# Kernel optimization log

Measured on AMD Instinct MI355X. Metric: run time of the kernel, lower is better.

## Reference

```python
import jax, jax.numpy as jnp
import numpy as np

HIDDEN = 1024
FFN = 4096
N_EXPERTS = 8
TOP_K = 2


def setup_inputs() -> dict:
    key = jax.random.key(0)
    ks = jax.random.split(key, 6)
    x = jax.random.normal(ks[0], (2, 2048, HIDDEN), dtype=jnp.float32)
    Wr = jax.random.normal(ks[1], (N_EXPERTS, HIDDEN), dtype=jnp.float32) * 0.02
    W1 = jax.random.normal(ks[2], (N_EXPERTS, FFN, HIDDEN), dtype=jnp.float32) * 0.02
    b1 = jnp.zeros((N_EXPERTS, FFN), dtype=jnp.float32)
    W2 = jax.random.normal(ks[3], (N_EXPERTS, HIDDEN, FFN), dtype=jnp.float32) * 0.02
    b2 = jnp.zeros((N_EXPERTS, HIDDEN), dtype=jnp.float32)
    return {"x": x, "Wr": Wr, "W1": W1, "b1": b1, "W2": W2, "b2": b2}


def reference(x, Wr, W1, b1, W2, b2):
    # x: [B, S, D]; Wr: [E, D]; W1: [E, F, D]; W2: [E, D, F]
    B, S, D = x.shape
    E = Wr.shape[0]
    xf = x.reshape(-1, D)                              # [T, D]
    T = xf.shape[0]
    logits = xf @ Wr.T                                 # [T, E]
    probs = jax.nn.softmax(logits, axis=-1)
    top_v, top_i = jax.lax.top_k(probs, TOP_K)         # [T, K]
    top_v = top_v / jnp.sum(top_v, axis=-1, keepdims=True)
    # combine weights: zero except the top-k experts per token
    comb = jnp.zeros((T, E), dtype=xf.dtype).at[jnp.arange(T)[:, None], top_i].add(top_v)
    # run every expert densely (same math as gather/FFN/weighted-scatter)
    h = jax.nn.gelu(jnp.einsum('td,efd->etf', xf, W1) + b1[:, None, :], approximate=False)  # [E, T, F]
    y = jnp.einsum('etf,edf->etd', h, W2) + b2[:, None, :]                                   # [E, T, D]
    out = jnp.einsum('etd,te->td', y, comb)            # weighted combine
    return out.reshape(B, S, D)
```

## Files before the change

### kernel.cpp

```cpp
#include <hip/hip_runtime.h>

#define HIDDEN 1024
#define FFN    4096
#define NEXP   8
#define TOKENS 4096
#define ASSIGN 8192

typedef __attribute__((ext_vector_type(8))) short s8v;
typedef __attribute__((ext_vector_type(4))) float f4v;

__device__ __forceinline__ float bf2f(ushort u) {
    return __uint_as_float(((unsigned int)u) << 16);
}
__device__ __forceinline__ ushort f2bf(float f) {
    unsigned int x = __float_as_uint(f);
    return (ushort)((x + 0x7fffu + ((x >> 16) & 1u)) >> 16);
}

#define GLDS16(g, l) __builtin_amdgcn_global_load_lds( \
    (const __attribute__((address_space(1))) unsigned int*)(g), \
    (__attribute__((address_space(3))) unsigned int*)(l), 16, 0, 0)

__device__ __forceinline__ int swz_scol(int t) {
    const int srow = t >> 2, c = t & 3;
    return ((c ^ ((srow >> 1) & 3)) << 3);
}
__device__ __forceinline__ int lds_off(int row, int lq) {
    return row * 32 + ((lq ^ ((row >> 1) & 3)) << 3);
}

__global__ void conv_kernel(const float4* __restrict__ src, ushort4* __restrict__ dst) {
    const int i = blockIdx.x * blockDim.x + threadIdx.x;
    const float4 v = src[i];
    ushort4 o;
    o.x = f2bf(v.x); o.y = f2bf(v.y); o.z = f2bf(v.z); o.w = f2bf(v.w);
    dst[i] = o;
}

__global__ void router_kernel(const float* __restrict__ x, const float* __restrict__ Wr,
                              int* __restrict__ counts, int* __restrict__ topk_idx,
                              float* __restrict__ topk_w) {
    const int tok  = blockIdx.x;
    const int lane = threadIdx.x;
    float acc[NEXP];
#pragma unroll
    for (int e = 0; e < NEXP; ++e) acc[e] = 0.f;
#pragma unroll
    for (int i = 0; i < HIDDEN / 64; ++i) {
        const int idx = i * 64 + lane;
        const float xv = x[(size_t)tok * HIDDEN + idx];
#pragma unroll
        for (int e = 0; e < NEXP; ++e) acc[e] += xv * Wr[e * HIDDEN + idx];
    }
#pragma unroll
    for (int e = 0; e < NEXP; ++e) {
#pragma unroll
        for (int off = 32; off > 0; off >>= 1) acc[e] += __shfl_xor(acc[e], off);
    }
    if (lane == 0) {
        int i0 = 0;
        for (int e = 1; e < NEXP; ++e) if (acc[e] > acc[i0]) i0 = e;
        int i1 = (i0 == 0) ? 1 : 0;
        for (int e = 0; e < NEXP; ++e) if (e != i0 && acc[e] > acc[i1]) i1 = e;
        const float e1 = expf(acc[i1] - acc[i0]);
        const float s  = 1.f + e1;
        topk_idx[tok * 2 + 0] = i0;
        topk_idx[tok * 2 + 1] = i1;
        topk_w[tok * 2 + 0]   = 1.f / s;
        topk_w[tok * 2 + 1]   = e1 / s;
        atomicAdd(&counts[i0], 1);
        atomicAdd(&counts[i1], 1);
    }
}

__global__ void prefix_kernel(const int* __restrict__ counts, int* __restrict__ offsets,
                              int* __restrict__ cursors) {
    if (threadIdx.x == 0) {
        int s = 0;
        for (int e = 0; e < NEXP; ++e) { offsets[e] = s; cursors[e] = s; s += counts[e]; }
        offsets[NEXP] = s;
    }
}

__global__ void scatter_kernel(const int* __restrict__ topk_idx, const float* __restrict__ topk_w,
                               int* __restrict__ cursors, int* __restrict__ token_list,
                               float* __restrict__ weight_list, int* __restrict__ slot_of) {
    const int a = blockIdx.x * blockDim.x + threadIdx.x;
    if (a >= ASSIGN) return;
    const int e   = topk_idx[a];
    const int pos = atomicAdd(&cursors[e], 1);
    token_list[pos]  = a >> 1;
    weight_list[pos] = topk_w[a];
    slot_of[a]       = pos;
}

__global__ __launch_bounds__(256)
void gemm1_kernel(const ushort* __restrict__ x, const ushort* __restrict__ W1,
                  const float* __restrict__ b1, const int* __restrict__ token_list,
                  const int* __restrict__ counts, const int* __restrict__ offsets,
                  ushort* __restrict__ h) {
    const int bid    = blockIdx.x;
    const int e      = bid & 7;
    const int r      = bid >> 3;
    const int tile_m = r & 63;
    const int tile_n = r >> 6;
    const int n_e    = counts[e];
    if (n_e <= 0 || tile_m * 128 >= n_e) return;
    const int base   = offsets[e];

    __shared__ __align__(16) ushort As[128 * 32];
    __shared__ __align__(16) ushort Bs[128 * 32];

    const int t    = threadIdx.x;
    const int lane = t & 63;
    const int wv   = t >> 6;
    const int srow = t >> 2;
    const int scol = swz_scol(t);

    const int r0 = tile_m * 128 + srow;
    const int r1 = r0 + 64;
    const int tokA0 = token_list[base + (r0 < n_e ? r0 : n_e - 1)];
    const int tokA1 = token_list[base + (r1 < n_e ? r1 : n_e - 1)];
    const ushort* gA0 = x + (size_t)tokA0 * HIDDEN + scol;
    const ushort* gA1 = x + (size_t)tokA1 * HIDDEN + scol;
    const ushort* gB0 = W1 + ((size_t)e * FFN + tile_n * 128 + srow) * HIDDEN + scol;
    const ushort* gB1 = W1 + ((size_t)e * FFN + tile_n * 128 + 64 + srow) * HIDDEN + scol;

    ushort* lA0 = As + wv * 512;
    ushort* lA1 = As + 2048 + wv * 512;
    ushort* lB0 = Bs + wv * 512;
    ushort* lB1 = Bs + 2048 + wv * 512;

    f4v acc[4][4];
#pragma unroll
    for (int i = 0; i < 4; ++i)
#pragma unroll
        for (int j = 0; j < 4; ++j) { f4v z = {0.f, 0.f, 0.f, 0.f}; acc[i][j] = z; }

    const int row_off = (wv & 1) * 64;
    const int col_off = (wv >> 1) * 64;
    const int l15 = lane & 15;
    const int lq  = lane >> 4;

    for (int k0 = 0; k0 < HIDDEN; k0 += 32) {
        GLDS16(gA0 + k0, lA0);
        GLDS16(gA1 + k0, lA1);
        GLDS16(gB0 + k0, lB0);
        GLDS16(gB1 + k0, lB1);
        __syncthreads();
        s8v a[4], b[4];
#pragma unroll
        for (int i = 0; i < 4; ++i) a[i] = *(const s8v*)(As + lds_off(row_off + i * 16 + l15, lq));
#pragma unroll
        for (int j = 0; j < 4; ++j) b[j] = *(const s8v*)(Bs + lds_off(col_off + j * 16 + l15, lq));
#pragma unroll
        for (int i = 0; i < 4; ++i)
#pragma unroll
            for (int j = 0; j < 4; ++j)
                acc[i][j] = __builtin_amdgcn_mfma_f32_16x16x32_bf16(a[i], b[j], acc[i][j], 0, 0, 0);
        __syncthreads();
    }

    const int mrem = n_e - tile_m * 128;
#pragma unroll
    for (int i = 0; i < 4; ++i) {
#pragma unroll
        for (int rr = 0; rr < 4; ++rr) {
            const int m_loc = row_off + i * 16 + lq * 4 + rr;
            if (m_loc < mrem) {
                const size_t hrow = (size_t)(base + tile_m * 128 + m_loc) * FFN;
#pragma unroll
                for (int j = 0; j < 4; ++j) {
                    const int colF = tile_n * 128 + col_off + j * 16 + l15;
                    float v = acc[i][j][rr] + b1[e * FFN + colF];
                    v = 0.5f * v * (1.0f + erff(v * 0.70710678118654752f));
                    h[hrow + colF] = f2bf(v);
                }
            }
        }
    }
}

__global__ __launch_bounds__(256)
void gemm2_kernel(const ushort* __restrict__ h, const ushort* __restrict__ W2,
                  const float* __restrict__ b2, const float* __restrict__ weight_list,
                  const int* __restrict__ counts, const int* __restrict__ offsets,
                  ushort* __restrict__ y) {
    const int bid    = blockIdx.x;
    const int e      = bid & 7;
    const int r      = bid >> 3;
    const int tile_m = r & 63;
    const int tile_n = r >> 6;
    const int n_e    = counts[e];
    if (n_e <= 0 || tile_m * 128 >= n_e) return;
    const int base   = offsets[e];

    __shared__ __align__(16) ushort As[128 * 32];
    __shared__ __align__(16) ushort Bs[64 * 32];

    const int t    = threadIdx.x;
    const int lane = t & 63;
    const int wv   = t >> 6;
    const int srow = t >> 2;
    const int scol = swz_scol(t);

    const int r0 = tile_m * 128 + srow;
    const int r1 = r0 + 64;
    const int slot0 = base + (r0 < n_e ? r0 : n_e - 1);
    const int slot1 = base + (r1 < n_e ? r1 : n_e - 1);
    const ushort* gA0 = h + (size_t)slot0 * FFN + scol;
    const ushort* gA1 = h + (size_t)slot1 * FFN + scol;
    const ushort* gB  = W2 + ((size_t)e * HIDDEN + tile_n * 64 + srow) * FFN + scol;

    ushort* lA0 = As + wv * 512;
    ushort* lA1 = As + 2048 + wv * 512;
    ushort* lB  = Bs + wv * 512;

    f4v acc[4][2];
#pragma unroll
    for (int i = 0; i < 4; ++i)
#pragma unroll
        for (int j = 0; j < 2; ++j) { f4v z = {0.f, 0.f, 0.f, 0.f}; acc[i][j] = z; }

    const int row_off = (wv & 1) * 64;
    const int col_off = (wv >> 1) * 32;
    const int l15 = lane & 15;
    const int lq  = lane >> 4;

    for (int k0 = 0; k0 < FFN; k0 += 32) {
        GLDS16(gA0 + k0, lA0);
        GLDS16(gA1 + k0, lA1);
        GLDS16(gB  + k0, lB);
        __syncthreads();
        s8v a[4], b[2];
#pragma unroll
        for (int i = 0; i < 4; ++i) a[i] = *(const s8v*)(As + lds_off(row_off + i * 16 + l15, lq));
#pragma unroll
        for (int j = 0; j < 2; ++j) b[j] = *(const s8v*)(Bs + lds_off(col_off + j * 16 + l15, lq));
#pragma unroll
        for (int i = 0; i < 4; ++i)
#pragma unroll
            for (int j = 0; j < 2; ++j)
                acc[i][j] = __builtin_amdgcn_mfma_f32_16x16x32_bf16(a[i], b[j], acc[i][j], 0, 0, 0);
        __syncthreads();
    }

    const int mrem = n_e - tile_m * 128;
#pragma unroll
    for (int i = 0; i < 4; ++i) {
#pragma unroll
        for (int rr = 0; rr < 4; ++rr) {
            const int m_loc = row_off + i * 16 + lq * 4 + rr;
            if (m_loc < mrem) {
                const int slot = base + tile_m * 128 + m_loc;
                const float wgt = weight_list[slot];
#pragma unroll
                for (int j = 0; j < 2; ++j) {
                    const int colD = tile_n * 64 + col_off + j * 16 + l15;
                    const float v = acc[i][j][rr] + b2[e * HIDDEN + colD];
                    y[(size_t)slot * HIDDEN + colD] = f2bf(v * wgt);
                }
            }
        }
    }
}

__global__ void combine_kernel(const int* __restrict__ slot_of, const ushort* __restrict__ y,
                               float* __restrict__ out) {
    const int idx = blockIdx.x * blockDim.x + threadIdx.x;
    const int t = idx >> 8;
    const int d = (idx & 255) * 4;
    const int s0 = slot_of[t * 2 + 0];
    const int s1 = slot_of[t * 2 + 1];
    const ushort4 a = *(const ushort4*)(y + (size_t)s0 * HIDDEN + d);
    const ushort4 b = *(const ushort4*)(y + (size_t)s1 * HIDDEN + d);
    float4 o;
    o.x = bf2f(a.x) + bf2f(b.x);
    o.y = bf2f(a.y) + bf2f(b.y);
    o.z = bf2f(a.z) + bf2f(b.z);
    o.w = bf2f(a.w) + bf2f(b.w);
    *(float4*)(out + (size_t)t * HIDDEN + d) = o;
}

extern "C" void kernel_launch(void* const* d_in, const int* in_sizes, int n_in,
                              void* d_out, int out_size, void* d_ws, size_t ws_size,
                              hipStream_t stream) {
    const float* x  = (const float*)d_in[0];
    const float* Wr = (const float*)d_in[1];
    const float* W1 = (const float*)d_in[2];
    const float* b1 = (const float*)d_in[3];
    const float* W2 = (const float*)d_in[4];
    const float* b2 = (const float*)d_in[5];
    float* out = (float*)d_out;

    char* ws = (char*)d_ws;
    int*    counts      = (int*)(ws + 0);
    int*    offsets     = (int*)(ws + 256);
    int*    cursors     = (int*)(ws + 512);
    int*    topk_idx    = (int*)(ws + 1024);
    float*  topk_w      = (float*)(ws + 1024 + 32768);
    int*    slot_of     = (int*)(ws + 1024 + 65536);
    int*    token_list  = (int*)(ws + 1024 + 98304);
    float*  weight_list = (float*)(ws + 1024 + 131072);
    ushort* x_bf        = (ushort*)(ws + (1 << 20));
    ushort* wbuf        = (ushort*)(ws + (1 << 20) + 8388608);
    ushort* h           = (ushort*)(ws + (1 << 20) + 8388608 + 67108864);
    ushort* y           = (ushort*)(ws + (1 << 20) + 8388608 + 2 * 67108864ull);

    const int NW = NEXP * FFN * HIDDEN;

    hipMemsetAsync(counts, 0, 64, stream);
    conv_kernel<<<(TOKENS * HIDDEN / 4) / 256, 256, 0, stream>>>((const float4*)x, (ushort4*)x_bf);
    conv_kernel<<<(NW / 4) / 256, 256, 0, stream>>>((const float4*)W1, (ushort4*)wbuf);

    router_kernel<<<TOKENS, 64, 0, stream>>>(x, Wr, counts, topk_idx, topk_w);
    prefix_kernel<<<1, 64, 0, stream>>>(counts, offsets, cursors);
    scatter_kernel<<<ASSIGN / 256, 256, 0, stream>>>(topk_idx, topk_w, cursors,
                                                     token_list, weight_list, slot_of);

    gemm1_kernel<<<NEXP * 64 * (FFN / 128), 256, 0, stream>>>(
        x_bf, wbuf, b1, token_list, counts, offsets, h);

    conv_kernel<<<(NW / 4) / 256, 256, 0, stream>>>((const float4*)W2, (ushort4*)wbuf);

    gemm2_kernel<<<NEXP * 64 * (HIDDEN / 64), 256, 0, stream>>>(
        h, wbuf, b2, weight_list, counts, offsets, y);

    combine_kernel<<<(TOKENS * HIDDEN / 4) / 256, 256, 0, stream>>>(slot_of, y, out);
}
```

Before: 749.1 us.

## Double K-step to 64 and widen gemm2 N tile to 128

Both expert GEMMs now stage 64-wide K slices per iteration with an 8-chunk XOR swizzle, halving barrier and loop overhead per MFMA. gemm2 grows its output tile from 128x64 to 128x128, so each wave holds a 4x4 accumulator grid and A-tile loads are reused across twice as many columns. This doubles LDS use per block and raises register pressure, which may reduce occupancy, and gemm2 launches half as many blocks.

```diff
diff --git a/kernel.cpp b/kernel.cpp
--- a/kernel.cpp
+++ b/kernel.cpp
@@ -22,11 +22,7 @@
     (__attribute__((address_space(3))) unsigned int*)(l), 16, 0, 0)
 
 __device__ __forceinline__ int swz_scol(int t) {
-    const int srow = t >> 2, c = t & 3;
-    return ((c ^ ((srow >> 1) & 3)) << 3);
-}
-__device__ __forceinline__ int lds_off(int row, int lq) {
-    return row * 32 + ((lq ^ ((row >> 1) & 3)) << 3);
+    return (((t & 7) ^ ((t >> 3) & 7)) << 3);
 }
 
 __global__ void conv_kernel(const float4* __restrict__ src, ushort4* __restrict__ dst) {
@@ -108,28 +104,29 @@
     if (n_e <= 0 || tile_m * 128 >= n_e) return;
     const int base   = offsets[e];
 
-    __shared__ __align__(16) ushort As[128 * 32];
-    __shared__ __align__(16) ushort Bs[128 * 32];
+    __shared__ __align__(16) ushort As[128 * 64];
+    __shared__ __align__(16) ushort Bs[128 * 64];
 
     const int t    = threadIdx.x;
     const int lane = t & 63;
     const int wv   = t >> 6;
-    const int srow = t >> 2;
+    const int srow = t >> 3;
     const int scol = swz_scol(t);
 
-    const int r0 = tile_m * 128 + srow;
-    const int r1 = r0 + 64;
-    const int tokA0 = token_list[base + (r0 < n_e ? r0 : n_e - 1)];
-    const int tokA1 = token_list[base + (r1 < n_e ? r1 : n_e - 1)];
-    const ushort* gA0 = x + (size_t)tokA0 * HIDDEN + scol;
-    const ushort* gA1 = x + (size_t)tokA1 * HIDDEN + scol;
-    const ushort* gB0 = W1 + ((size_t)e * FFN + tile_n * 128 + srow) * HIDDEN + scol;
-    const ushort* gB1 = W1 + ((size_t)e * FFN + tile_n * 128 + 64 + srow) * HIDDEN + scol;
-
-    ushort* lA0 = As + wv * 512;
-    ushort* lA1 = As + 2048 + wv * 512;
-    ushort* lB0 = Bs + wv * 512;
-    ushort* lB1 = Bs + 2048 + wv * 512;
+    const ushort* gA[4];
+#pragma unroll
+    for (int c = 0; c < 4; ++c) {
+        const int rr  = tile_m * 128 + c * 32 + srow;
+        const int tok = token_list[base + (rr < n_e ? rr : n_e - 1)];
+        gA[c] = x + (size_t)tok * HIDDEN + scol;
+    }
+    const ushort* gB[4];
+#pragma unroll
+    for (int c = 0; c < 4; ++c)
+        gB[c] = W1 + ((size_t)e * FFN + tile_n * 128 + c * 32 + srow) * HIDDEN + scol;
+
+    ushort* lA = As + wv * 512;
+    ushort* lB = Bs + wv * 512;
 
     f4v acc[4][4];
 #pragma unroll
@@ -141,23 +138,28 @@
     const int col_off = (wv >> 1) * 64;
     const int l15 = lane & 15;
     const int lq  = lane >> 4;
-
-    for (int k0 = 0; k0 < HIDDEN; k0 += 32) {
-        GLDS16(gA0 + k0, lA0);
-        GLDS16(gA1 + k0, lA1);
-        GLDS16(gB0 + k0, lB0);
-        GLDS16(gB1 + k0, lB1);
+    const int rx  = l15 & 7;
+
+    for (int k0 = 0; k0 < HIDDEN; k0 += 64) {
+#pragma unroll
+        for (int c = 0; c < 4; ++c) GLDS16(gA[c] + k0, lA + c * 2048);
+#pragma unroll
+        for (int c = 0; c < 4; ++c) GLDS16(gB[c] + k0, lB + c * 2048);
         __syncthreads();
-        s8v a[4], b[4];
-#pragma unroll
-        for (int i = 0; i < 4; ++i) a[i] = *(const s8v*)(As + lds_off(row_off + i * 16 + l15, lq));
-#pragma unroll
-        for (int j = 0; j < 4; ++j) b[j] = *(const s8v*)(Bs + lds_off(col_off + j * 16 + l15, lq));
-#pragma unroll
-        for (int i = 0; i < 4; ++i)
-#pragma unroll
-            for (int j = 0; j < 4; ++j)
-                acc[i][j] = __builtin_amdgcn_mfma_f32_16x16x32_bf16(a[i], b[j], acc[i][j], 0, 0, 0);
+#pragma unroll
+        for (int kk = 0; kk < 2; ++kk) {
+            const int co = (((kk << 2) | lq) ^ rx) << 3;
+            s8v a[4], b[4];
+#pragma unroll
+            for (int i = 0; i < 4; ++i) a[i] = *(const s8v*)(As + (row_off + i * 16 + l15) * 64 + co);
+#pragma unroll
+            for (int j = 0; j < 4; ++j) b[j] = *(const s8v*)(Bs + (col_off + j * 16 + l15) * 64 + co);
+#pragma unroll
+            for (int i = 0; i < 4; ++i)
+#pragma unroll
+                for (int j = 0; j < 4; ++j)
+                    acc[i][j] = __builtin_amdgcn_mfma_f32_16x16x32_bf16(a[i], b[j], acc[i][j], 0, 0, 0);
+        }
         __syncthreads();
     }
 
@@ -195,53 +197,62 @@
     if (n_e <= 0 || tile_m * 128 >= n_e) return;
     const int base   = offsets[e];
 
-    __shared__ __align__(16) ushort As[128 * 32];
-    __shared__ __align__(16) ushort Bs[64 * 32];
+    __shared__ __align__(16) ushort As[128 * 64];
+    __shared__ __align__(16) ushort Bs[128 * 64];
 
     const int t    = threadIdx.x;
     const int lane = t & 63;
     const int wv   = t >> 6;
-    const int srow = t >> 2;
+    const int srow = t >> 3;
     const int scol = swz_scol(t);
 
-    const int r0 = tile_m * 128 + srow;
-    const int r1 = r0 + 64;
-    const int slot0 = base + (r0 < n_e ? r0 : n_e - 1);
-    const int slot1 = base + (r1 < n_e ? r1 : n_e - 1);
-    const ushort* gA0 = h + (size_t)slot0 * FFN + scol;
-    const ushort* gA1 = h + (size_t)slot1 * FFN + scol;
-    const ushort* gB  = W2 + ((size_t)e * HIDDEN + tile_n * 64 + srow) * FFN + scol;
-
-    ushort* lA0 = As + wv * 512;
-    ushort* lA1 = As + 2048 + wv * 512;
-    ushort* lB  = Bs + wv * 512;
-
-    f4v acc[4][2];
+    const ushort* gA[4];
+#pragma unroll
+    for (int c = 0; c < 4; ++c) {
+        const int rr = tile_m * 128 + c * 32 + srow;
+        const int slot = base + (rr < n_e ? rr : n_e - 1);
+        gA[c] = h + (size_t)slot * FFN + scol;
+    }
+    const ushort* gB[4];
+#pragma unroll
+    for (int c = 0; c < 4; ++c)
+        gB[c] = W2 + ((size_t)e * HIDDEN + tile_n * 128 + c * 32 + srow) * FFN + scol;
+
+    ushort* lA = As + wv * 512;
+    ushort* lB = Bs + wv * 512;
+
+    f4v acc[4][4];
 #pragma unroll
     for (int i = 0; i < 4; ++i)
 #pragma unroll
-        for (int j = 0; j < 2; ++j) { f4v z = {0.f, 0.f, 0.f, 0.f}; acc[i][j] = z; }
+        for (int j = 0; j < 4; ++j) { f4v z = {0.f, 0.f, 0.f, 0.f}; acc[i][j] = z; }
 
     const int row_off = (wv & 1) * 64;
-    const int col_off = (wv >> 1) * 32;
+    const int col_off = (wv >> 1) * 64;
     const int l15 = lane & 15;
     const int lq  = lane >> 4;
-
-    for (int k0 = 0; k0 < FFN; k0 += 32) {
-        GLDS16(gA0 + k0, lA0);
-        GLDS16(gA1 + k0, lA1);
-        GLDS16(gB  + k0, lB);
+    const int rx  = l15 & 7;
+
+    for (int k0 = 0; k0 < FFN; k0 += 64) {
+#pragma unroll
+        for (int c = 0; c < 4; ++c) GLDS16(gA[c] + k0, lA + c * 2048);
+#pragma unroll
+        for (int c = 0; c < 4; ++c) GLDS16(gB[c] + k0, lB + c * 2048);
         __syncthreads();
-        s8v a[4], b[2];
-#pragma unroll
-        for (int i = 0; i < 4; ++i) a[i] = *(const s8v*)(As + lds_off(row_off + i * 16 + l15, lq));
-#pragma unroll
-        for (int j = 0; j < 2; ++j) b[j] = *(const s8v*)(Bs + lds_off(col_off + j * 16 + l15, lq));
-#pragma unroll
-        for (int i = 0; i < 4; ++i)
-#pragma unroll
-            for (int j = 0; j < 2; ++j)
-                acc[i][j] = __builtin_amdgcn_mfma_f32_16x16x32_bf16(a[i], b[j], acc[i][j], 0, 0, 0);
+#pragma unroll
+        for (int kk = 0; kk < 2; ++kk) {
+            const int co = (((kk << 2) | lq) ^ rx) << 3;
+            s8v a[4], b[4];
+#pragma unroll
+            for (int i = 0; i < 4; ++i) a[i] = *(const s8v*)(As + (row_off + i * 16 + l15) * 64 + co);
+#pragma unroll
+            for (int j = 0; j < 4; ++j) b[j] = *(const s8v*)(Bs + (col_off + j * 16 + l15) * 64 + co);
+#pragma unroll
+            for (int i = 0; i < 4; ++i)
+#pragma unroll
+                for (int j = 0; j < 4; ++j)
+                    acc[i][j] = __builtin_amdgcn_mfma_f32_16x16x32_bf16(a[i], b[j], acc[i][j], 0, 0, 0);
+        }
         __syncthreads();
     }
 
@@ -255,8 +266,8 @@
                 const int slot = base + tile_m * 128 + m_loc;
                 const float wgt = weight_list[slot];
 #pragma unroll
-                for (int j = 0; j < 2; ++j) {
-                    const int colD = tile_n * 64 + col_off + j * 16 + l15;
+                for (int j = 0; j < 4; ++j) {
+                    const int colD = tile_n * 128 + col_off + j * 16 + l15;
                     const float v = acc[i][j][rr] + b2[e * HIDDEN + colD];
                     y[(size_t)slot * HIDDEN + colD] = f2bf(v * wgt);
                 }
@@ -323,7 +334,7 @@
 
     conv_kernel<<<(NW / 4) / 256, 256, 0, stream>>>((const float4*)W2, (ushort4*)wbuf);
 
-    gemm2_kernel<<<NEXP * 64 * (HIDDEN / 64), 256, 0, stream>>>(
+    gemm2_kernel<<<NEXP * 64 * (HIDDEN / 128), 256, 0, stream>>>(
         h, wbuf, b2, weight_list, counts, offsets, y);
 
     combine_kernel<<<(TOKENS * HIDDEN / 4) / 256, 256, 0, stream>>>(slot_of, y, out);
```

Result: slower. 772.2 us (+3.1%).

## Double-buffer LDS in both expert GEMMs and widen gemm2 tile to 128x128

Applied to the files above, without the earlier changes.

Both grouped GEMM kernels now keep two LDS buffers. The next K-slice is fetched with global_load_lds while MFMAs consume the current one, which removes the second barrier per iteration. gemm2's N tile grows from 64 to 128 so each wave computes a 4x4 MFMA block, matching gemm1, and the grid is halved. This raises LDS use to 32 KB per block and adds accumulator registers, which may reduce occupancy, and gemm2 now has fewer blocks to spread across CUs.

```diff
diff --git a/kernel.cpp b/kernel.cpp
--- a/kernel.cpp
+++ b/kernel.cpp
@@ -108,8 +108,8 @@
     if (n_e <= 0 || tile_m * 128 >= n_e) return;
     const int base   = offsets[e];
 
-    __shared__ __align__(16) ushort As[128 * 32];
-    __shared__ __align__(16) ushort Bs[128 * 32];
+    __shared__ __align__(16) ushort As[2 * 128 * 32];
+    __shared__ __align__(16) ushort Bs[2 * 128 * 32];
 
     const int t    = threadIdx.x;
     const int lane = t & 63;
@@ -126,11 +126,6 @@
     const ushort* gB0 = W1 + ((size_t)e * FFN + tile_n * 128 + srow) * HIDDEN + scol;
     const ushort* gB1 = W1 + ((size_t)e * FFN + tile_n * 128 + 64 + srow) * HIDDEN + scol;
 
-    ushort* lA0 = As + wv * 512;
-    ushort* lA1 = As + 2048 + wv * 512;
-    ushort* lB0 = Bs + wv * 512;
-    ushort* lB1 = Bs + 2048 + wv * 512;
-
     f4v acc[4][4];
 #pragma unroll
     for (int i = 0; i < 4; ++i)
@@ -142,23 +137,36 @@
     const int l15 = lane & 15;
     const int lq  = lane >> 4;
 
-    for (int k0 = 0; k0 < HIDDEN; k0 += 32) {
-        GLDS16(gA0 + k0, lA0);
-        GLDS16(gA1 + k0, lA1);
-        GLDS16(gB0 + k0, lB0);
-        GLDS16(gB1 + k0, lB1);
+    GLDS16(gA0, As + wv * 512);
+    GLDS16(gA1, As + 2048 + wv * 512);
+    GLDS16(gB0, Bs + wv * 512);
+    GLDS16(gB1, Bs + 2048 + wv * 512);
+
+    int cur = 0;
+    for (int it = 0; it < HIDDEN / 32; ++it) {
         __syncthreads();
+        if (it + 1 < HIDDEN / 32) {
+            const int kn = (it + 1) * 32;
+            ushort* dA = As + (cur ^ 1) * 4096 + wv * 512;
+            ushort* dB = Bs + (cur ^ 1) * 4096 + wv * 512;
+            GLDS16(gA0 + kn, dA);
+            GLDS16(gA1 + kn, dA + 2048);
+            GLDS16(gB0 + kn, dB);
+            GLDS16(gB1 + kn, dB + 2048);
+        }
+        const ushort* bA = As + cur * 4096;
+        const ushort* bB = Bs + cur * 4096;
         s8v a[4], b[4];
 #pragma unroll
-        for (int i = 0; i < 4; ++i) a[i] = *(const s8v*)(As + lds_off(row_off + i * 16 + l15, lq));
-#pragma unroll
-        for (int j = 0; j < 4; ++j) b[j] = *(const s8v*)(Bs + lds_off(col_off + j * 16 + l15, lq));
+        for (int i = 0; i < 4; ++i) a[i] = *(const s8v*)(bA + lds_off(row_off + i * 16 + l15, lq));
+#pragma unroll
+        for (int j = 0; j < 4; ++j) b[j] = *(const s8v*)(bB + lds_off(col_off + j * 16 + l15, lq));
 #pragma unroll
         for (int i = 0; i < 4; ++i)
 #pragma unroll
             for (int j = 0; j < 4; ++j)
                 acc[i][j] = __builtin_amdgcn_mfma_f32_16x16x32_bf16(a[i], b[j], acc[i][j], 0, 0, 0);
-        __syncthreads();
+        cur ^= 1;
     }
 
     const int mrem = n_e - tile_m * 128;
@@ -195,8 +203,8 @@
     if (n_e <= 0 || tile_m * 128 >= n_e) return;
     const int base   = offsets[e];
 
-    __shared__ __align__(16) ushort As[128 * 32];
-    __shared__ __align__(16) ushort Bs[64 * 32];
+    __shared__ __align__(16) ushort As[2 * 128 * 32];
+    __shared__ __align__(16) ushort Bs[2 * 128 * 32];
 
     const int t    = threadIdx.x;
     const int lane = t & 63;
@@ -210,39 +218,50 @@
     const int slot1 = base + (r1 < n_e ? r1 : n_e - 1);
     const ushort* gA0 = h + (size_t)slot0 * FFN + scol;
     const ushort* gA1 = h + (size_t)slot1 * FFN + scol;
-    const ushort* gB  = W2 + ((size_t)e * HIDDEN + tile_n * 64 + srow) * FFN + scol;
-
-    ushort* lA0 = As + wv * 512;
-    ushort* lA1 = As + 2048 + wv * 512;
-    ushort* lB  = Bs + wv * 512;
-
-    f4v acc[4][2];
+    const ushort* gB0 = W2 + ((size_t)e * HIDDEN + tile_n * 128 + srow) * FFN + scol;
+    const ushort* gB1 = W2 + ((size_t)e * HIDDEN + tile_n * 128 + 64 + srow) * FFN + scol;
+
+    f4v acc[4][4];
 #pragma unroll
     for (int i = 0; i < 4; ++i)
 #pragma unroll
-        for (int j = 0; j < 2; ++j) { f4v z = {0.f, 0.f, 0.f, 0.f}; acc[i][j] = z; }
+        for (int j = 0; j < 4; ++j) { f4v z = {0.f, 0.f, 0.f, 0.f}; acc[i][j] = z; }
 
     const int row_off = (wv & 1) * 64;
-    const int col_off = (wv >> 1) * 32;
+    const int col_off = (wv >> 1) * 64;
     const int l15 = lane & 15;
     const int lq  = lane >> 4;
 
-    for (int k0 = 0; k0 < FFN; k0 += 32) {
-        GLDS16(gA0 + k0, lA0);
-        GLDS16(gA1 + k0, lA1);
-        GLDS16(gB  + k0, lB);
+    GLDS16(gA0, As + wv * 512);
+    GLDS16(gA1, As + 2048 + wv * 512);
+    GLDS16(gB0, Bs + wv * 512);
+    GLDS16(gB1, Bs + 2048 + wv * 512);
+
+    int cur = 0;
+    for (int it = 0; it < FFN / 32; ++it) {
         __syncthreads();
-        s8v a[4], b[2];
-#pragma unroll
-        for (int i = 0; i < 4; ++i) a[i] = *(const s8v*)(As + lds_off(row_off + i * 16 + l15, lq));
-#pragma unroll
-        for (int j = 0; j < 2; ++j) b[j] = *(const s8v*)(Bs + lds_off(col_off + j * 16 + l15, lq));
+        if (it + 1 < FFN / 32) {
+            const int kn = (it + 1) * 32;
+            ushort* dA = As + (cur ^ 1) * 4096 + wv * 512;
+            ushort* dB = Bs + (cur ^ 1) * 4096 + wv * 512;
+            GLDS16(gA0 + kn, dA);
+            GLDS16(gA1 + kn, dA + 2048);
+            GLDS16(gB0 + kn, dB);
+            GLDS16(gB1 + kn, dB + 2048);
+        }
+        const ushort* bA = As + cur * 4096;
+        const ushort* bB = Bs + cur * 4096;
+        s8v a[4], b[4];
+#pragma unroll
+        for (int i = 0; i < 4; ++i) a[i] = *(const s8v*)(bA + lds_off(row_off + i * 16 + l15, lq));
+#pragma unroll
+        for (int j = 0; j < 4; ++j) b[j] = *(const s8v*)(bB + lds_off(col_off + j * 16 + l15, lq));
 #pragma unroll
         for (int i = 0; i < 4; ++i)
 #pragma unroll
-            for (int j = 0; j < 2; ++j)
+            for (int j = 0; j < 4; ++j)
                 acc[i][j] = __builtin_amdgcn_mfma_f32_16x16x32_bf16(a[i], b[j], acc[i][j], 0, 0, 0);
-        __syncthreads();
+        cur ^= 1;
     }
 
     const int mrem = n_e - tile_m * 128;
@@ -255,8 +274,8 @@
                 const int slot = base + tile_m * 128 + m_loc;
                 const float wgt = weight_list[slot];
 #pragma unroll
-                for (int j = 0; j < 2; ++j) {
-                    const int colD = tile_n * 64 + col_off + j * 16 + l15;
+                for (int j = 0; j < 4; ++j) {
+                    const int colD = tile_n * 128 + col_off + j * 16 + l15;
                     const float v = acc[i][j][rr] + b2[e * HIDDEN + colD];
                     y[(size_t)slot * HIDDEN + colD] = f2bf(v * wgt);
                 }
@@ -323,7 +342,7 @@
 
     conv_kernel<<<(NW / 4) / 256, 256, 0, stream>>>((const float4*)W2, (ushort4*)wbuf);
 
-    gemm2_kernel<<<NEXP * 64 * (HIDDEN / 64), 256, 0, stream>>>(
+    gemm2_kernel<<<NEXP * 64 * (HIDDEN / 128), 256, 0, stream>>>(
         h, wbuf, b2, weight_list, counts, offsets, y);
 
     combine_kernel<<<(TOKENS * HIDDEN / 4) / 256, 256, 0, stream>>>(slot_of, y, out);
```

New measurement: 733.7 us. -2.1%, faster.

## Triple-buffer LDS prefetch in both expert GEMMs and widen gemm2 tile

Applied to the files above, without the earlier changes.

Both expert GEMM kernels now keep three LDS stages. Loads for the tile two steps ahead are issued asynchronously, and a vmcnt wait plus a single barrier per step replaces the load/sync/compute/sync pattern. The goal is to hide global-to-LDS latency behind MFMA work. gemm2 also moves from a 128x64 to a 128x128 output tile, which halves its grid and improves reuse of the activation tile. The cost is more LDS per block (48KB), which may limit occupancy, and the vmcnt count must match the per-thread load order.

```diff
diff --git a/kernel.cpp b/kernel.cpp
--- a/kernel.cpp
+++ b/kernel.cpp
@@ -28,6 +28,34 @@
 __device__ __forceinline__ int lds_off(int row, int lq) {
     return row * 32 + ((lq ^ ((row >> 1) & 3)) << 3);
 }
+
+#define KBODY(it, bA, bB, sA, sB)                                               \
+  {                                                                             \
+    if ((it) == NT - 1) { asm volatile("s_waitcnt vmcnt(0)" ::: "memory"); }    \
+    else                { asm volatile("s_waitcnt vmcnt(4)" ::: "memory"); }    \
+    __builtin_amdgcn_s_barrier();                                               \
+    __builtin_amdgcn_sched_barrier(0);                                          \
+    if ((it) + 2 < NT) {                                                        \
+      const int kn_ = ((it) + 2) * 32;                                          \
+      GLDS16(gA0 + kn_, (sA) + wv * 512);                                       \
+      GLDS16(gA1 + kn_, (sA) + 2048 + wv * 512);                                \
+      GLDS16(gB0 + kn_, (sB) + wv * 512);                                       \
+      GLDS16(gB1 + kn_, (sB) + 2048 + wv * 512);                                \
+    }                                                                           \
+    s8v a_[4], b_[4];                                                           \
+    _Pragma("unroll")                                                           \
+    for (int i_ = 0; i_ < 4; ++i_)                                              \
+      a_[i_] = *(const s8v*)((bA) + lds_off(row_off + i_ * 16 + l15, lq));      \
+    _Pragma("unroll")                                                           \
+    for (int j_ = 0; j_ < 4; ++j_)                                              \
+      b_[j_] = *(const s8v*)((bB) + lds_off(col_off + j_ * 16 + l15, lq));      \
+    _Pragma("unroll")                                                           \
+    for (int i_ = 0; i_ < 4; ++i_)                                              \
+      _Pragma("unroll")                                                         \
+      for (int j_ = 0; j_ < 4; ++j_)                                            \
+        acc[i_][j_] = __builtin_amdgcn_mfma_f32_16x16x32_bf16(a_[i_], b_[j_],   \
+                                                              acc[i_][j_], 0, 0, 0); \
+  }
 
 __global__ void conv_kernel(const float4* __restrict__ src, ushort4* __restrict__ dst) {
     const int i = blockIdx.x * blockDim.x + threadIdx.x;
@@ -108,8 +136,8 @@
     if (n_e <= 0 || tile_m * 128 >= n_e) return;
     const int base   = offsets[e];
 
-    __shared__ __align__(16) ushort As[128 * 32];
-    __shared__ __align__(16) ushort Bs[128 * 32];
+    __shared__ __align__(16) ushort As[3 * 128 * 32];
+    __shared__ __align__(16) ushort Bs[3 * 128 * 32];
 
     const int t    = threadIdx.x;
     const int lane = t & 63;
@@ -126,11 +154,6 @@
     const ushort* gB0 = W1 + ((size_t)e * FFN + tile_n * 128 + srow) * HIDDEN + scol;
     const ushort* gB1 = W1 + ((size_t)e * FFN + tile_n * 128 + 64 + srow) * HIDDEN + scol;
 
-    ushort* lA0 = As + wv * 512;
-    ushort* lA1 = As + 2048 + wv * 512;
-    ushort* lB0 = Bs + wv * 512;
-    ushort* lB1 = Bs + 2048 + wv * 512;
-
     f4v acc[4][4];
 #pragma unroll
     for (int i = 0; i < 4; ++i)
@@ -142,23 +165,21 @@
     const int l15 = lane & 15;
     const int lq  = lane >> 4;
 
-    for (int k0 = 0; k0 < HIDDEN; k0 += 32) {
-        GLDS16(gA0 + k0, lA0);
-        GLDS16(gA1 + k0, lA1);
-        GLDS16(gB0 + k0, lB0);
-        GLDS16(gB1 + k0, lB1);
-        __syncthreads();
-        s8v a[4], b[4];
-#pragma unroll
-        for (int i = 0; i < 4; ++i) a[i] = *(const s8v*)(As + lds_off(row_off + i * 16 + l15, lq));
-#pragma unroll
-        for (int j = 0; j < 4; ++j) b[j] = *(const s8v*)(Bs + lds_off(col_off + j * 16 + l15, lq));
-#pragma unroll
-        for (int i = 0; i < 4; ++i)
-#pragma unroll
-            for (int j = 0; j < 4; ++j)
-                acc[i][j] = __builtin_amdgcn_mfma_f32_16x16x32_bf16(a[i], b[j], acc[i][j], 0, 0, 0);
-        __syncthreads();
+    const int NT = HIDDEN / 32;
+
+    GLDS16(gA0,      As + wv * 512);
+    GLDS16(gA1,      As + 2048 + wv * 512);
+    GLDS16(gB0,      Bs + wv * 512);
+    GLDS16(gB1,      Bs + 2048 + wv * 512);
+    GLDS16(gA0 + 32, As + 4096 + wv * 512);
+    GLDS16(gA1 + 32, As + 4096 + 2048 + wv * 512);
+    GLDS16(gB0 + 32, Bs + 4096 + wv * 512);
+    GLDS16(gB1 + 32, Bs + 4096 + 2048 + wv * 512);
+
+    for (int it0 = 0; it0 < NT; it0 += 3) {
+        KBODY(it0,     As,        Bs,        As + 8192, Bs + 8192);
+        if (it0 + 1 < NT) KBODY(it0 + 1, As + 4096, Bs + 4096, As,        Bs);
+        if (it0 + 2 < NT) KBODY(it0 + 2, As + 8192, Bs + 8192, As + 4096, Bs + 4096);
     }
 
     const int mrem = n_e - tile_m * 128;
@@ -195,8 +216,8 @@
     if (n_e <= 0 || tile_m * 128 >= n_e) return;
     const int base   = offsets[e];
 
-    __shared__ __align__(16) ushort As[128 * 32];
-    __shared__ __align__(16) ushort Bs[64 * 32];
+    __shared__ __align__(16) ushort As[3 * 128 * 32];
+    __shared__ __align__(16) ushort Bs[3 * 128 * 32];
 
     const int t    = threadIdx.x;
     const int lane = t & 63;
@@ -210,39 +231,35 @@
     const int slot1 = base + (r1 < n_e ? r1 : n_e - 1);
     const ushort* gA0 = h + (size_t)slot0 * FFN + scol;
     const ushort* gA1 = h + (size_t)slot1 * FFN + scol;
-    const ushort* gB  = W2 + ((size_t)e * HIDDEN + tile_n * 64 + srow) * FFN + scol;
-
-    ushort* lA0 = As + wv * 512;
-    ushort* lA1 = As + 2048 + wv * 512;
-    ushort* lB  = Bs + wv * 512;
-
-    f4v acc[4][2];
+    const ushort* gB0 = W2 + ((size_t)e * HIDDEN + tile_n * 128 + srow) * FFN + scol;
+    const ushort* gB1 = W2 + ((size_t)e * HIDDEN + tile_n * 128 + 64 + srow) * FFN + scol;
+
+    f4v acc[4][4];
 #pragma unroll
     for (int i = 0; i < 4; ++i)
 #pragma unroll
-        for (int j = 0; j < 2; ++j) { f4v z = {0.f, 0.f, 0.f, 0.f}; acc[i][j] = z; }
+        for (int j = 0; j < 4; ++j) { f4v z = {0.f, 0.f, 0.f, 0.f}; acc[i][j] = z; }
 
     const int row_off = (wv & 1) * 64;
-    const int col_off = (wv >> 1) * 32;
+    const int col_off = (wv >> 1) * 64;
     const int l15 = lane & 15;
     const int lq  = lane >> 4;
 
-    for (int k0 = 0; k0 < FFN; k0 += 32) {
-        GLDS16(gA0 + k0, lA0);
-        GLDS16(gA1 + k0, lA1);
-        GLDS16(gB  + k0, lB);
-        __syncthreads();
-        s8v a[4], b[2];
-#pragma unroll
-        for (int i = 0; i < 4; ++i) a[i] = *(const s8v*)(As + lds_off(row_off + i * 16 + l15, lq));
-#pragma unroll
-        for (int j = 0; j < 2; ++j) b[j] = *(const s8v*)(Bs + lds_off(col_off + j * 16 + l15, lq));
-#pragma unroll
-        for (int i = 0; i < 4; ++i)
-#pragma unroll
-            for (int j = 0; j < 2; ++j)
-                acc[i][j] = __builtin_amdgcn_mfma_f32_16x16x32_bf16(a[i], b[j], acc[i][j], 0, 0, 0);
-        __syncthreads();
+    const int NT = FFN / 32;
+
+    GLDS16(gA0,      As + wv * 512);
+    GLDS16(gA1,      As + 2048 + wv * 512);
+    GLDS16(gB0,      Bs + wv * 512);
+    GLDS16(gB1,      Bs + 2048 + wv * 512);
+    GLDS16(gA0 + 32, As + 4096 + wv * 512);
+    GLDS16(gA1 + 32, As + 4096 + 2048 + wv * 512);
+    GLDS16(gB0 + 32, Bs + 4096 + wv * 512);
+    GLDS16(gB1 + 32, Bs + 4096 + 2048 + wv * 512);
+
+    for (int it0 = 0; it0 < NT; it0 += 3) {
+        KBODY(it0,     As,        Bs,        As + 8192, Bs + 8192);
+        if (it0 + 1 < NT) KBODY(it0 + 1, As + 4096, Bs + 4096, As,        Bs);
+        if (it0 + 2 < NT) KBODY(it0 + 2, As + 8192, Bs + 8192, As + 4096, Bs + 4096);
     }
 
     const int mrem = n_e - tile_m * 128;
@@ -255,8 +272,8 @@
                 const int slot = base + tile_m * 128 + m_loc;
                 const float wgt = weight_list[slot];
 #pragma unroll
-                for (int j = 0; j < 2; ++j) {
-                    const int colD = tile_n * 64 + col_off + j * 16 + l15;
+                for (int j = 0; j < 4; ++j) {
+                    const int colD = tile_n * 128 + col_off + j * 16 + l15;
                     const float v = acc[i][j][rr] + b2[e * HIDDEN + colD];
                     y[(size_t)slot * HIDDEN + colD] = f2bf(v * wgt);
                 }
@@ -323,7 +340,7 @@
 
     conv_kernel<<<(NW / 4) / 256, 256, 0, stream>>>((const float4*)W2, (ushort4*)wbuf);
 
-    gemm2_kernel<<<NEXP * 64 * (HIDDEN / 64), 256, 0, stream>>>(
+    gemm2_kernel<<<NEXP * 64 * (HIDDEN / 128), 256, 0, stream>>>(
         h, wbuf, b2, weight_list, counts, offsets, y);
 
     combine_kernel<<<(TOKENS * HIDDEN / 4) / 256, 256, 0, stream>>>(slot_of, y, out);
```

Result: faster. 696.3 us (-7.1%).
